# Optimization experiments

Measured on AMD Instinct MI355X. Metric: run time of the kernel, lower is better.

Reference implementation:

```python
import jax, jax.numpy as jnp
import numpy as np
import math

L, D, NH, HD, H, V = 6, 384, 6, 64, 768, 4096
B, T = 4, 2048


def setup_inputs() -> dict:
    key = jax.random.key(0)
    ks = jax.random.split(key, 16)
    s = 0.02
    inp = {
        "x": jax.random.randint(ks[0], (B, T), 0, V, dtype=jnp.int32),
        "emb": jax.random.normal(ks[1], (V, D), jnp.float32) * s,
        "wq": jax.random.normal(ks[2], (L, D, D), jnp.float32) * s,
        "wk": jax.random.normal(ks[3], (L, D, D), jnp.float32) * s,
        "wv": jax.random.normal(ks[4], (L, D, D), jnp.float32) * s,
        "wo": jax.random.normal(ks[5], (L, D, D), jnp.float32) * s,
        "ln1": jnp.ones((L, D), jnp.float32),
        "ln2": jnp.ones((L, D), jnp.float32),
        "w1": jax.random.normal(ks[6], (L, D, H), jnp.float32) * s,
        "b1": jnp.zeros((L, H), jnp.float32),
        "w2": jax.random.normal(ks[7], (L, H, D), jnp.float32) * s,
        "b2": jnp.zeros((L, D), jnp.float32),
        "lnf": jnp.ones((D,), jnp.float32),
        "head": jax.random.normal(ks[8], (D, V), jnp.float32) * s,
    }
    return inp


def _rms(x, w):
    return x * jax.lax.rsqrt(jnp.mean(x * x, axis=-1, keepdims=True) + 1e-6) * w


def _attn(x, wq, wk, wv, wo):
    b, t, _ = x.shape
    q = (x @ wq).reshape(b, t, NH, HD).transpose(0, 2, 1, 3)  # [b,h,t,hd]
    k = (x @ wk).reshape(b, t, NH, HD).transpose(0, 2, 1, 3)
    v = (x @ wv).reshape(b, t, NH, HD).transpose(0, 2, 1, 3)
    scores = jnp.einsum('bhqd,bhkd->bhqk', q, k) / math.sqrt(HD)
    causal = jnp.tril(jnp.ones((t, t), bool))
    scores = jnp.where(causal, scores, -jnp.inf)
    a = jax.nn.softmax(scores, axis=-1)
    o = jnp.einsum('bhqk,bhkd->bhqd', a, v)
    o = o.transpose(0, 2, 1, 3).reshape(b, t, D)
    return o @ wo


def reference(x, emb, wq, wk, wv, wo, ln1, ln2, w1, b1, w2, b2, lnf, head):
    h = emb[x]  # [B,T,D]
    mid = None
    for i in range(L):
        h = h + _attn(_rms(h, ln1[i]), wq[i], wk[i], wv[i], wo[i])
        hn = _rms(h, ln2[i])
        ff = jax.nn.gelu(hn @ w1[i] + b1[i], approximate=False) @ w2[i] + b2[i]
        h = h + ff
        if i == 2:
            mid = h
    logits = _rms(h, lnf) @ head
    return logits, mid
```

## Files before the change

kernel.cpp:

```cpp
#include <hip/hip_runtime.h>
#include <hip/hip_bf16.h>
#include <math.h>

#define L_  6
#define D_  384
#define NH_ 6
#define HD_ 64
#define HF_ 768
#define V_  4096
#define B_  4
#define T_  2048
#define BT_ (B_*T_)

typedef unsigned short u16;
typedef __attribute__((ext_vector_type(8))) short short8;
typedef __attribute__((ext_vector_type(4))) float f32x4;

__device__ __forceinline__ float bf2f(u16 u){
  union { unsigned int i; float f; } c; c.i = ((unsigned int)u)<<16; return c.f;
}
__device__ __forceinline__ u16 f2bf(float f){
  union { float f; unsigned int i; } c; c.f = f;
  unsigned int x = c.i;
  x += 0x7fffu + ((x>>16)&1u);
  return (u16)(x>>16);
}
__device__ __forceinline__ f32x4 mfma16(short8 a, short8 b, f32x4 c){
  return __builtin_amdgcn_mfma_f32_16x16x32_bf16(a,b,c,0,0,0);
}
template<int CTRL>
__device__ __forceinline__ float dppmax(float x){
  int v = __builtin_amdgcn_update_dpp(0, __builtin_bit_cast(int, x), CTRL, 0xf, 0xf, true);
  return fmaxf(x, __builtin_bit_cast(float, v));
}
__device__ __forceinline__ float rowmax16(float x){
  x = dppmax<0xB1>(x);
  x = dppmax<0x4E>(x);
  x = dppmax<0x141>(x);
  x = dppmax<0x140>(x);
  return x;
}
#define GLD16(gp, lp) __builtin_amdgcn_global_load_lds( \
    (const __attribute__((address_space(1))) void*)(gp), \
    (__attribute__((address_space(3))) void*)(lp), 16, 0, 0)

__global__ void embed_kernel(const int* __restrict__ x, const float* __restrict__ emb,
                             float* __restrict__ h){
  const int idx = blockIdx.x*256 + threadIdx.x;
  if(idx >= BT_*D_) return;
  const int t = idx / D_;
  const int d = idx - t*D_;
  h[idx] = emb[(size_t)x[t]*D_ + d];
}

__global__ __launch_bounds__(256) void wtrans_kernel(const float* __restrict__ src,
    u16* __restrict__ dst, int K, int N, size_t srcBatch, size_t dstBatch){
  __shared__ float tile[32][33];
  src += (size_t)blockIdx.z*srcBatch;
  dst += (size_t)blockIdx.z*dstBatch;
  const int tx = threadIdx.x&31, ty = threadIdx.x>>5;
  const int n0 = blockIdx.x*32, k0 = blockIdx.y*32;
  #pragma unroll
  for(int j=0;j<4;j++)
    tile[ty+j*8][tx] = src[(size_t)(k0+ty+j*8)*N + n0+tx];
  __syncthreads();
  #pragma unroll
  for(int j=0;j<4;j++)
    dst[(size_t)(n0+ty+j*8)*K + k0+tx] = f2bf(tile[tx][ty+j*8]);
}

__global__ __launch_bounds__(256) void rms_kernel(const float* __restrict__ h,
                                                  const float* __restrict__ w,
                                                  u16* __restrict__ out){
  const int wave = threadIdx.x>>6, lane = threadIdx.x&63;
  const size_t row = (size_t)blockIdx.x*4 + wave;
  const float* hr = h + row*D_;
  float v[6]; float ss = 0.f;
  #pragma unroll
  for(int i=0;i<6;i++){ v[i] = hr[lane + i*64]; ss += v[i]*v[i]; }
  #pragma unroll
  for(int o=1;o<64;o<<=1) ss += __shfl_xor(ss, o);
  const float rn = rsqrtf(ss*(1.f/D_) + 1e-6f);
  u16* orow = out + row*D_;
  #pragma unroll
  for(int i=0;i<6;i++) orow[lane+i*64] = f2bf(v[i]*rn*w[lane+i*64]);
}

__global__ void copy_kernel(const float* __restrict__ src, float* __restrict__ dst, int n){
  const int i = blockIdx.x*256 + threadIdx.x;
  if(i < n) dst[i] = src[i];
}

template<int MODE, int K, int BN>
__global__ __launch_bounds__(256) void gemm_kernel(
    const u16* __restrict__ A, const u16* __restrict__ Wt, int N,
    const float* __restrict__ bias, u16* __restrict__ out, float* __restrict__ fout,
    u16* __restrict__ qo, u16* __restrict__ ko, u16* __restrict__ vo)
{
  __shared__ u16 As[128*64];
  __shared__ u16 Bs[BN*64];
  const int w = threadIdx.x>>6, lane = threadIdx.x&63;
  const int l16 = lane&15, quad = lane>>4;
  const int r0 = blockIdx.y*128, n0 = blockIdx.x*BN;
  const int mst = lane>>3;
  const int cst = (lane&7) ^ (lane>>3);

  constexpr int MI = (BN==128) ? 4 : 2;
  const int wrow = (BN==128) ? (w&1)*64 : w*32;
  const int wcol = (BN==128) ? (w>>1)*64 : 0;

  f32x4 acc[MI][4];
  #pragma unroll
  for(int mi=0;mi<MI;mi++)
    #pragma unroll
    for(int ni=0;ni<4;ni++){ acc[mi][ni][0]=0.f; acc[mi][ni][1]=0.f; acc[mi][ni][2]=0.f; acc[mi][ni][3]=0.f; }

  for(int k0=0;k0<K;k0+=64){
    __syncthreads();
    #pragma unroll
    for(int i=0;i<4;i++){
      const int m = (w*4+i)*8 + mst;
      GLD16(A + (size_t)(r0+m)*K + k0 + cst*8, As + (size_t)(w*4+i)*512);
    }
    if constexpr(BN==128){
      #pragma unroll
      for(int i=0;i<4;i++){
        const int n = (w*4+i)*8 + mst;
        GLD16(Wt + (size_t)(n0+n)*K + k0 + cst*8, Bs + (size_t)(w*4+i)*512);
      }
    } else {
      #pragma unroll
      for(int i=0;i<2;i++){
        const int n = (w*2+i)*8 + mst;
        GLD16(Wt + (size_t)(n0+n)*K + k0 + cst*8, Bs + (size_t)(w*2+i)*512);
      }
    }
    asm volatile("s_waitcnt vmcnt(0)" ::: "memory");
    __syncthreads();
    #pragma unroll
    for(int ks=0;ks<2;ks++){
      short8 av[MI], bv[4];
      #pragma unroll
      for(int mi=0;mi<MI;mi++){
        const int m = wrow + mi*16 + l16;
        av[mi] = *(const short8*)&As[m*64 + (((ks*4+quad)^(l16&7))*8)];
      }
      #pragma unroll
      for(int ni=0;ni<4;ni++){
        const int n = wcol + ni*16 + l16;
        bv[ni] = *(const short8*)&Bs[n*64 + (((ks*4+quad)^(l16&7))*8)];
      }
      #pragma unroll
      for(int mi=0;mi<MI;mi++)
        #pragma unroll
        for(int ni=0;ni<4;ni++)
          acc[mi][ni] = mfma16(av[mi], bv[ni], acc[mi][ni]);
    }
  }

  #pragma unroll
  for(int mi=0;mi<MI;mi++){
    #pragma unroll
    for(int ni=0;ni<4;ni++){
      const int col = n0 + wcol + ni*16 + l16;
      #pragma unroll
      for(int r=0;r<4;r++){
        const int row = r0 + wrow + mi*16 + quad*4 + r;
        float v = acc[mi][ni][r];
        if(MODE==0){
          fout[(size_t)row*N + col] = v;
        } else if(MODE==1){
          v += bias[col];
          v = 0.5f*v*(1.f + erff(v*0.70710678118f));
          out[(size_t)row*N + col] = f2bf(v);
        } else if(MODE==2){
          if(bias) v += bias[col];
          fout[(size_t)row*N + col] += v;
        } else {
          if(col < D_)        qo[(size_t)row*D_ + col]      = f2bf(v);
          else if(col < 2*D_) ko[(size_t)row*D_ + (col-D_)] = f2bf(v);
          else {
            const int cv = col - 2*D_;
            const int hh = cv>>6, dd = cv&63;
            const int bb = row>>11, tt = row&(T_-1);
            vo[(((size_t)(bb*NH_+hh))*HD_ + dd)*T_ + tt] = f2bf(v);
          }
        }
      }
    }
  }
}

__global__ __launch_bounds__(256) void flash_kernel(const u16* __restrict__ q,
    const u16* __restrict__ k, const u16* __restrict__ vt, u16* __restrict__ ao){
  __shared__ u16 Ks[2][64*64];
  __shared__ u16 Vs[2][80*64];
  __shared__ __align__(16) u16 Pb[4][16*64];
  const int tid = threadIdx.x;
  const int w = tid>>6, lane = tid&63;
  const int l16 = lane&15, quad = lane>>4;
  const int bh = blockIdx.y, b = bh/NH_, h = bh - b*NH_;
  const int qt = (gridDim.x-1) - blockIdx.x;
  const int qw = qt*64 + w*16;

  {
    const int idx0 = tid*8;
    #pragma unroll
    for(int i=0;i<8;i++){
      const int idx = idx0 + i;
      const int bu = idx>>10, rem = idx&1023;
      Vs[bu][(64 + (rem>>6))*64 + (rem&63)] = ((rem>>6)==0) ? (u16)0x3F80 : (u16)0;
    }
  }
  __syncthreads();

  const u16* qp = q + ((size_t)(b*T_ + qw + l16))*D_ + h*HD_ + quad*8;
  short8 qf0 = *(const short8*)(qp);
  short8 qf1 = *(const short8*)(qp + 32);

  const u16* kbase = k + (size_t)(b*T_)*D_ + h*HD_;
  const u16* vbase = vt + (size_t)(b*NH_ + h)*HD_*T_;
  u16* Pw = &Pb[w][0];

  const int srow = lane>>3;
  const int schunk = lane&7;
  const int kgc = schunk ^ srow;

  float m[4];
  f32x4 o[5];
  #pragma unroll
  for(int r=0;r<4;r++) m[r] = -1e30f;
  #pragma unroll
  for(int c=0;c<5;c++){ o[c][0]=0.f; o[c][1]=0.f; o[c][2]=0.f; o[c][3]=0.f; }

  const int nkt = qt + 1;

  #pragma unroll
  for(int i=0;i<2;i++){
    const int j = w*2+i;
    GLD16(kbase + (size_t)(j*8 + srow)*D_ + kgc*8, &Ks[0][j*512]);
  }
  #pragma unroll
  for(int i=0;i<2;i++){
    const int j = w*2+i;
    GLD16(vbase + (size_t)(j*8 + srow)*T_ + (schunk^srow)*8, &Vs[0][j*512]);
  }

  for(int kt=0; kt<nkt; kt++){
    const u16* Kc = Ks[kt&1];
    const u16* Vc = Vs[kt&1];
    if(kt+1 < nkt){
      const int kb2 = (kt+1)*64;
      #pragma unroll
      for(int i=0;i<2;i++){
        const int j = w*2+i;
        GLD16(kbase + (size_t)(kb2 + j*8 + srow)*D_ + kgc*8, &Ks[(kt+1)&1][j*512]);
      }
      #pragma unroll
      for(int i=0;i<2;i++){
        const int j = w*2+i;
        GLD16(vbase + (size_t)(j*8 + srow)*T_ + kb2 + (schunk^srow)*8, &Vs[(kt+1)&1][j*512]);
      }
      asm volatile("s_waitcnt vmcnt(4)" ::: "memory");
    } else {
      asm volatile("s_waitcnt vmcnt(0)" ::: "memory");
    }
    __builtin_amdgcn_s_barrier();

    float s[4][4];
    __builtin_amdgcn_s_setprio(1);
    #pragma unroll
    for(int c=0;c<4;c++){
      const int krow = c*16 + l16;
      short8 kf0 = *(const short8*)&Kc[krow*64 + ((quad^(l16&7))*8)];
      short8 kf1 = *(const short8*)&Kc[krow*64 + (((4+quad)^(l16&7))*8)];
      f32x4 sa = {0.f,0.f,0.f,0.f};
      sa = mfma16(qf0, kf0, sa);
      sa = mfma16(qf1, kf1, sa);
      #pragma unroll
      for(int r=0;r<4;r++) s[c][r] = sa[r]*0.125f;
    }
    __builtin_amdgcn_s_setprio(0);
    if(kt == nkt-1){
      const int kb = kt*64;
      #pragma unroll
      for(int c=0;c<4;c++){
        const int kpos = kb + c*16 + l16;
        #pragma unroll
        for(int r=0;r<4;r++)
          if(kpos > qw + quad*4 + r) s[c][r] = -1e30f;
      }
    }
    float tmr[4];
    #pragma unroll
    for(int r=0;r<4;r++){
      float tm = fmaxf(fmaxf(s[0][r], s[1][r]), fmaxf(s[2][r], s[3][r]));
      tmr[r] = rowmax16(tm);
    }
    float need = tmr[0] - m[0];
    #pragma unroll
    for(int r=1;r<4;r++) need = fmaxf(need, tmr[r] - m[r]);
    if(!__all(need <= 8.f)){
      #pragma unroll
      for(int r=0;r<4;r++){
        const float mn = fmaxf(m[r], tmr[r]);
        const float al = __expf(m[r] - mn);
        #pragma unroll
        for(int c=0;c<5;c++) o[c][r] *= al;
        m[r] = mn;
      }
    }
    #pragma unroll
    for(int r=0;r<4;r++){
      const int prow = quad*4 + r;
      #pragma unroll
      for(int c=0;c<4;c++){
        const float p = __expf(s[c][r] - m[r]);
        Pw[prow*64 + (((c*2 + (l16>>3)) ^ (prow&7))<<3) + (l16&7)] = f2bf(p);
      }
    }
    __builtin_amdgcn_s_setprio(1);
    #pragma unroll
    for(int kk=0;kk<2;kk++){
      short8 pf = *(const short8*)&Pw[l16*64 + (((kk*4+quad) ^ (l16&7))<<3)];
      #pragma unroll
      for(int c=0;c<5;c++){
        const int dd = c*16 + l16;
        short8 vf = *(const short8*)&Vc[dd*64 + (((kk*4+quad)^(l16&7))<<3)];
        o[c] = mfma16(pf, vf, o[c]);
      }
    }
    __builtin_amdgcn_s_setprio(0);
    __builtin_amdgcn_s_barrier();
  }
  #pragma unroll
  for(int r=0;r<4;r++){
    const float lr = __shfl(o[4][r], quad<<4, 64);
    const float il = 1.f / lr;
    const size_t row = (size_t)(b*T_ + qw + quad*4 + r);
    #pragma unroll
    for(int c=0;c<4;c++)
      ao[row*D_ + h*HD_ + c*16 + l16] = f2bf(o[c][r] * il);
  }
}

extern "C" void kernel_launch(void* const* d_in, const int* in_sizes, int n_in,
                              void* d_out, int out_size, void* d_ws, size_t ws_size,
                              hipStream_t stream) {
  const int*   x    = (const int*)d_in[0];
  const float* emb  = (const float*)d_in[1];
  const float* wq   = (const float*)d_in[2];
  const float* wk   = (const float*)d_in[3];
  const float* wv   = (const float*)d_in[4];
  const float* wo   = (const float*)d_in[5];
  const float* ln1  = (const float*)d_in[6];
  const float* ln2  = (const float*)d_in[7];
  const float* w1   = (const float*)d_in[8];
  const float* b1   = (const float*)d_in[9];
  const float* w2   = (const float*)d_in[10];
  const float* b2   = (const float*)d_in[11];
  const float* lnf  = (const float*)d_in[12];
  const float* head = (const float*)d_in[13];
  float* out = (float*)d_out;

  char* ws = (char*)d_ws; size_t off = 0;
  auto alloc = [&](size_t bytes)->void* {
    void* p = ws + off; off += (bytes + 255) & ~(size_t)255; return p;
  };
  float* hbuf  = (float*)alloc((size_t)BT_*D_*4);
  u16* xn    = (u16*)alloc((size_t)BT_*D_*2);
  u16* qb    = (u16*)alloc((size_t)BT_*D_*2);
  u16* kb    = (u16*)alloc((size_t)BT_*D_*2);
  u16* vtb   = (u16*)alloc((size_t)BT_*D_*2);
  u16* aob   = (u16*)alloc((size_t)BT_*D_*2);
  u16* midb  = (u16*)alloc((size_t)BT_*HF_*2);
  u16* qkvt  = (u16*)alloc((size_t)L_*3*D_*D_*2);
  u16* wot   = (u16*)alloc((size_t)L_*D_*D_*2);
  u16* w1t   = (u16*)alloc((size_t)L_*HF_*D_*2);
  u16* w2t   = (u16*)alloc((size_t)L_*D_*HF_*2);
  u16* headt = (u16*)alloc((size_t)V_*D_*2);

  const dim3 blk(256);
  wtrans_kernel<<<dim3(D_/32, D_/32, L_), blk, 0, stream>>>(wq, qkvt,           D_, D_, (size_t)D_*D_, (size_t)3*D_*D_);
  wtrans_kernel<<<dim3(D_/32, D_/32, L_), blk, 0, stream>>>(wk, qkvt + D_*D_,   D_, D_, (size_t)D_*D_, (size_t)3*D_*D_);
  wtrans_kernel<<<dim3(D_/32, D_/32, L_), blk, 0, stream>>>(wv, qkvt + 2*D_*D_, D_, D_, (size_t)D_*D_, (size_t)3*D_*D_);
  wtrans_kernel<<<dim3(D_/32, D_/32, L_), blk, 0, stream>>>(wo, wot,            D_, D_, (size_t)D_*D_, (size_t)D_*D_);
  wtrans_kernel<<<dim3(HF_/32, D_/32, L_), blk, 0, stream>>>(w1, w1t, D_, HF_, (size_t)D_*HF_, (size_t)HF_*D_);
  wtrans_kernel<<<dim3(D_/32, HF_/32, L_), blk, 0, stream>>>(w2, w2t, HF_, D_, (size_t)D_*HF_, (size_t)D_*HF_);
  wtrans_kernel<<<dim3(V_/32, D_/32, 1),  blk, 0, stream>>>(head, headt, D_, V_, 0, 0);

  embed_kernel<<<(BT_*D_ + 255)/256, blk, 0, stream>>>(x, emb, hbuf);

  for(int li=0; li<L_; li++){
    rms_kernel<<<BT_/4, blk, 0, stream>>>(hbuf, ln1 + li*D_, xn);
    gemm_kernel<3,D_,128><<<dim3(3*D_/128, BT_/128), blk, 0, stream>>>(
        xn, qkvt + (size_t)li*3*D_*D_, 3*D_, nullptr, nullptr, nullptr, qb, kb, vtb);
    flash_kernel<<<dim3(T_/64, B_*NH_), blk, 0, stream>>>(qb, kb, vtb, aob);
    gemm_kernel<2,D_,64><<<dim3(D_/64, BT_/128), blk, 0, stream>>>(
        aob, wot + (size_t)li*D_*D_, D_, nullptr, nullptr, hbuf, nullptr, nullptr, nullptr);
    rms_kernel<<<BT_/4, blk, 0, stream>>>(hbuf, ln2 + li*D_, xn);
    gemm_kernel<1,D_,128><<<dim3(HF_/128, BT_/128), blk, 0, stream>>>(
        xn, w1t + (size_t)li*HF_*D_, HF_, b1 + li*HF_, midb, nullptr, nullptr, nullptr, nullptr);
    gemm_kernel<2,HF_,64><<<dim3(D_/64, BT_/128), blk, 0, stream>>>(
        midb, w2t + (size_t)li*D_*HF_, D_, b2 + li*D_, nullptr, hbuf, nullptr, nullptr, nullptr);
    if(li == 2)
      copy_kernel<<<(BT_*D_ + 255)/256, blk, 0, stream>>>(hbuf, out + (size_t)BT_*V_, BT_*D_);
  }
  rms_kernel<<<BT_/4, blk, 0, stream>>>(hbuf, lnf, xn);
  gemm_kernel<0,D_,128><<<dim3(V_/128, BT_/128), blk, 0, stream>>>(
      xn, headt, V_, nullptr, nullptr, out, nullptr, nullptr, nullptr);
}
```

Before: 1.224 ms.

## Double-buffer GEMM shared-memory tiles to overlap global loads with MFMA

Converts the GEMM main loop to a two-stage LDS pipeline: the next K-tile is issued with direct-to-LDS loads while the current tile is consumed, waiting only on the older loads via partial vmcnt counts. It also raises wave priority around the MFMA block. This targets exposed global-load latency per K step, in exchange for doubling LDS use per block, which may reduce occupancy. The hardcoded vmcnt values must match the number of loads issued per stage.

```diff
diff --git a/kernel.cpp b/kernel.cpp
--- a/kernel.cpp
+++ b/kernel.cpp
@@ -97,8 +97,8 @@
     const float* __restrict__ bias, u16* __restrict__ out, float* __restrict__ fout,
     u16* __restrict__ qo, u16* __restrict__ ko, u16* __restrict__ vo)
 {
-  __shared__ u16 As[128*64];
-  __shared__ u16 Bs[BN*64];
+  __shared__ u16 As[2][128*64];
+  __shared__ u16 Bs[2][BN*64];
   const int w = threadIdx.x>>6, lane = threadIdx.x&63;
   const int l16 = lane&15, quad = lane>>4;
   const int r0 = blockIdx.y*128, n0 = blockIdx.x*BN;
@@ -106,6 +106,7 @@
   const int cst = (lane&7) ^ (lane>>3);
 
   constexpr int MI = (BN==128) ? 4 : 2;
+  constexpr int NKT = K/64;
   const int wrow = (BN==128) ? (w&1)*64 : w*32;
   const int wcol = (BN==128) ? (w>>1)*64 : 0;
 
@@ -115,46 +116,66 @@
     #pragma unroll
     for(int ni=0;ni<4;ni++){ acc[mi][ni][0]=0.f; acc[mi][ni][1]=0.f; acc[mi][ni][2]=0.f; acc[mi][ni][3]=0.f; }
 
-  for(int k0=0;k0<K;k0+=64){
-    __syncthreads();
+  auto stage = [&](int kt, int bu){
+    const int k0 = kt*64;
     #pragma unroll
     for(int i=0;i<4;i++){
       const int m = (w*4+i)*8 + mst;
-      GLD16(A + (size_t)(r0+m)*K + k0 + cst*8, As + (size_t)(w*4+i)*512);
+      GLD16(A + (size_t)(r0+m)*K + k0 + cst*8, &As[bu][(w*4+i)*512]);
     }
     if constexpr(BN==128){
       #pragma unroll
       for(int i=0;i<4;i++){
         const int n = (w*4+i)*8 + mst;
-        GLD16(Wt + (size_t)(n0+n)*K + k0 + cst*8, Bs + (size_t)(w*4+i)*512);
+        GLD16(Wt + (size_t)(n0+n)*K + k0 + cst*8, &Bs[bu][(w*4+i)*512]);
       }
     } else {
       #pragma unroll
       for(int i=0;i<2;i++){
         const int n = (w*2+i)*8 + mst;
-        GLD16(Wt + (size_t)(n0+n)*K + k0 + cst*8, Bs + (size_t)(w*2+i)*512);
-      }
-    }
-    asm volatile("s_waitcnt vmcnt(0)" ::: "memory");
-    __syncthreads();
+        GLD16(Wt + (size_t)(n0+n)*K + k0 + cst*8, &Bs[bu][(w*2+i)*512]);
+      }
+    }
+  };
+
+  stage(0, 0);
+  for(int kt=0; kt<NKT; kt++){
+    const u16* Ac = As[kt&1];
+    const u16* Bc = Bs[kt&1];
+    if(kt+1 < NKT){
+      stage(kt+1, (kt+1)&1);
+      if constexpr(BN==128) asm volatile("s_waitcnt vmcnt(8)" ::: "memory");
+      else                  asm volatile("s_waitcnt vmcnt(6)" ::: "memory");
+    } else {
+      asm volatile("s_waitcnt vmcnt(0)" ::: "memory");
+    }
+    __builtin_amdgcn_s_barrier();
+    asm volatile("" ::: "memory");
+
+    __builtin_amdgcn_s_setprio(1);
     #pragma unroll
     for(int ks=0;ks<2;ks++){
       short8 av[MI], bv[4];
       #pragma unroll
       for(int mi=0;mi<MI;mi++){
         const int m = wrow + mi*16 + l16;
-        av[mi] = *(const short8*)&As[m*64 + (((ks*4+quad)^(l16&7))*8)];
+        av[mi] = *(const short8*)&Ac[m*64 + (((ks*4+quad)^(l16&7))*8)];
       }
       #pragma unroll
       for(int ni=0;ni<4;ni++){
         const int n = wcol + ni*16 + l16;
-        bv[ni] = *(const short8*)&Bs[n*64 + (((ks*4+quad)^(l16&7))*8)];
+        bv[ni] = *(const short8*)&Bc[n*64 + (((ks*4+quad)^(l16&7))*8)];
       }
       #pragma unroll
       for(int mi=0;mi<MI;mi++)
         #pragma unroll
         for(int ni=0;ni<4;ni++)
           acc[mi][ni] = mfma16(av[mi], bv[ni], acc[mi][ni]);
+    }
+    __builtin_amdgcn_s_setprio(0);
+    if(kt+1 < NKT){
+      asm volatile("" ::: "memory");
+      __builtin_amdgcn_s_barrier();
     }
   }
 
```

New measurement: 1.205 ms. About the same (-1.6%).
